# Kernel tuning notes

Hardware: AMD Instinct MI355X
Metric: run time of the kernel (lower is better)

Reference implementation:

```python
import jax, jax.numpy as jnp
import numpy as np

B, N, D = 16, 4096, 128
M = 2048  # codebook size
EPS = 1e-10


def setup_inputs() -> dict:
    key = jax.random.key(0)
    kx, kw = jax.random.split(key)
    x = jax.random.normal(kx, (B, N, D), dtype=jnp.float32)
    # codebook (nn.Embedding weight, kaiming-uniform init ~ uniform(-bound, bound))
    bound = np.sqrt(6.0 / D)
    weight = jax.random.uniform(kw, (M, D), dtype=jnp.float32, minval=-bound, maxval=bound)
    return {"x": x, "weight": weight}


def reference(x, weight):
    b, n, d = x.shape
    m = weight.shape[0]
    q = x.reshape(b * n, d)                       # (bn, d)
    # squared L2 distances: ||q||^2 + ||k||^2 - 2 q.k  (temperature==0 -> argmax of -dist)
    l2_q = jnp.sum(q * q, axis=1, keepdims=True)  # (bn, 1)
    l2_k = jnp.sum(weight * weight, axis=1)       # (m,)
    sim = q @ weight.T                            # (bn, m)  GEMM
    dist = l2_q + l2_k - 2.0 * sim
    indices = jnp.argmin(dist, axis=1)            # (bn,)
    z = weight[indices]                           # onehot @ k == gather
    quantized = z.reshape(b, n, d)
    # straight-through estimator (training path): q + (z - q).detach()
    quantized_st = x + jax.lax.stop_gradient(quantized - x)
    # commitment loss: mse(quantized.detach(), x)
    loss = jnp.mean((jax.lax.stop_gradient(quantized_st) - x) ** 2)
    # perplexity over codebook usage (h == 1 head)
    counts = jnp.zeros((m,), dtype=x.dtype).at[indices].add(1.0)
    p = counts / (b * n)                          # mean of onehot over (b, n)
    perp = jnp.exp(-jnp.sum(p * jnp.log(p + EPS)))[None]  # shape (1,) == 'h'
    out_indices = indices.reshape(b, 1, n)
    return quantized_st, loss, perp, out_indices
```

## Files before the change

### kernel.cpp

```cpp
#include <hip/hip_runtime.h>
#include <hip/hip_bf16.h>
#include <math.h>

#define D_DIM 128
#define M_CODES 2048
#define BN_TOT 65536
#define OUT_LOSS 8388608
#define OUT_PERP 8388609
#define OUT_IDX 8388610
#define MARGIN 2e-3f

#define QB 32

#define WS_L2K 0
#define WS_PHI 8192
#define WS_PLO 532480
#define WS_IDX 1056768
#define WS_PART 1318912
#define WS_CNT 1351680
#define WS_FLAGCNT 1359872
#define WS_FLAGGED 1360896

typedef __bf16 bf16x8 __attribute__((ext_vector_type(8)));
typedef float f32x4 __attribute__((ext_vector_type(4)));

#define A_STRIDE 136

__global__ __launch_bounds__(256) void l2_kernel(const float* __restrict__ w,
                                                 float* __restrict__ l2k) {
  int i = blockIdx.x * 256 + threadIdx.x;
  const float4* p = (const float4*)(w + (size_t)i * D_DIM);
  double s = 0.0;
#pragma unroll
  for (int j = 0; j < 32; ++j) {
    float4 v = p[j];
    s += (double)(v.x * v.x);
    s += (double)(v.y * v.y);
    s += (double)(v.z * v.z);
    s += (double)(v.w * v.w);
  }
  l2k[i] = (float)s;
}

__global__ __launch_bounds__(256) void pack_w_frag(const float* __restrict__ w,
                                                   __bf16* __restrict__ phi,
                                                   __bf16* __restrict__ plo) {
  int gid = blockIdx.x * 256 + threadIdx.x;
  int lane = gid & 63;
  int t = gid >> 6;
  int nt = t & 3;
  int ks = (t >> 2) & 3;
  int c64 = t >> 4;
  int code = c64 * 64 + nt * 16 + (lane & 15);
  int koff = ks * 32 + (lane >> 4) * 8;
  const float* src = w + (size_t)code * D_DIM + koff;
  float4 u = *(const float4*)src;
  float4 v = *(const float4*)(src + 4);
  float f[8] = {u.x, u.y, u.z, u.w, v.x, v.y, v.z, v.w};
  bf16x8 h, l;
#pragma unroll
  for (int j = 0; j < 8; ++j) {
    __bf16 hh = (__bf16)f[j];
    h[j] = hh;
    l[j] = (__bf16)(f[j] - (float)hh);
  }
  *(bf16x8*)(phi + (size_t)gid * 8) = h;
  *(bf16x8*)(plo + (size_t)gid * 8) = l;
}

__device__ __forceinline__ void merge_bs(float& b, float& s, int& i,
                                         float ob, float os, int oi) {
  if (ob < b) {
    s = fminf(b, os);
    b = ob;
    i = oi;
  } else if (ob > b) {
    s = fminf(s, ob);
  } else {
    s = b;
    if (oi < i) i = oi;
  }
}

__global__ __launch_bounds__(256, 1) void argmin_mfma(
    const float* __restrict__ x, const __bf16* __restrict__ phi,
    const __bf16* __restrict__ plo, const float* __restrict__ l2k,
    int* __restrict__ best_idx, int* __restrict__ flag_count,
    int* __restrict__ flagged) {
  __shared__ __bf16 aHi[QB * A_STRIDE];
  __shared__ __bf16 aLo[QB * A_STRIDE];
  __shared__ float redB[4][QB];
  __shared__ float redS[4][QB];
  __shared__ int redI[4][QB];

  const int tid = threadIdx.x;
  const int q0 = blockIdx.x * QB;
  const int wv = tid >> 6;
  const int lane = tid & 63;
  const int col = lane & 15;
  const int quad = lane >> 4;

#pragma unroll
  for (int it = 0; it < 4; ++it) {
    int fid = tid + it * 256;
    int q = fid >> 5;
    int k4 = (fid & 31) * 4;
    float4 v = *(const float4*)(x + (size_t)(q0 + q) * D_DIM + k4);
    float f[4] = {v.x, v.y, v.z, v.w};
    int base = q * A_STRIDE + k4;
#pragma unroll
    for (int j = 0; j < 4; ++j) {
      __bf16 h = (__bf16)f[j];
      aHi[base + j] = h;
      aLo[base + j] = (__bf16)(f[j] - (float)h);
    }
  }
  __syncthreads();

  float m1[2][4], m2[2][4];
  int bi[2][4];
#pragma unroll
  for (int mt = 0; mt < 2; ++mt)
#pragma unroll
    for (int r = 0; r < 4; ++r) {
      m1[mt][r] = 3.4e38f;
      m2[mt][r] = 3.4e38f;
      bi[mt][r] = 0;
    }

  for (int ch = 0; ch < 8; ++ch) {
    const int cb = ch * 256 + wv * 64;
    const int cb64 = ch * 4 + wv;

    bf16x8 bh[4][4], bl[4][4];
#pragma unroll
    for (int ks = 0; ks < 4; ++ks) {
#pragma unroll
      for (int nt = 0; nt < 4; ++nt) {
        size_t g = (((size_t)cb64 * 16) + ks * 4 + nt) * 64 + lane;
        bh[ks][nt] = *(const bf16x8*)(phi + g * 8);
        bl[ks][nt] = *(const bf16x8*)(plo + g * 8);
      }
    }

    f32x4 acc[2][4];
#pragma unroll
    for (int mt = 0; mt < 2; ++mt)
#pragma unroll
      for (int nt = 0; nt < 4; ++nt) acc[mt][nt] = (f32x4){0.f, 0.f, 0.f, 0.f};

#pragma unroll
    for (int ks = 0; ks < 4; ++ks) {
      bf16x8 ah[2], al[2];
#pragma unroll
      for (int mt = 0; mt < 2; ++mt) {
        int off = (16 * mt + col) * A_STRIDE + 32 * ks + quad * 8;
        ah[mt] = *(const bf16x8*)&aHi[off];
        al[mt] = *(const bf16x8*)&aLo[off];
      }
#pragma unroll
      for (int nt = 0; nt < 4; ++nt) {
#pragma unroll
        for (int mt = 0; mt < 2; ++mt) {
          acc[mt][nt] = __builtin_amdgcn_mfma_f32_16x16x32_bf16(
              al[mt], bh[ks][nt], acc[mt][nt], 0, 0, 0);
          acc[mt][nt] = __builtin_amdgcn_mfma_f32_16x16x32_bf16(
              ah[mt], bl[ks][nt], acc[mt][nt], 0, 0, 0);
          acc[mt][nt] = __builtin_amdgcn_mfma_f32_16x16x32_bf16(
              ah[mt], bh[ks][nt], acc[mt][nt], 0, 0, 0);
        }
      }
    }

#pragma unroll
    for (int nt = 0; nt < 4; ++nt) {
      int ci = cb + 16 * nt + col;
      float l2 = l2k[ci];
#pragma unroll
      for (int mt = 0; mt < 2; ++mt) {
#pragma unroll
        for (int r = 0; r < 4; ++r) {
          float dd = fmaf(-2.0f, acc[mt][nt][r], l2);
          bool lt = dd < m1[mt][r];
          m2[mt][r] = lt ? m1[mt][r] : fminf(m2[mt][r], dd);
          bi[mt][r] = lt ? ci : bi[mt][r];
          m1[mt][r] = fminf(m1[mt][r], dd);
        }
      }
    }
  }

#pragma unroll
  for (int mt = 0; mt < 2; ++mt) {
#pragma unroll
    for (int r = 0; r < 4; ++r) {
      float b = m1[mt][r], s = m2[mt][r];
      int i = bi[mt][r];
#pragma unroll
      for (int m = 1; m < 16; m <<= 1) {
        float ob = __shfl_xor(b, m);
        float os = __shfl_xor(s, m);
        int oi = __shfl_xor(i, m);
        merge_bs(b, s, i, ob, os, oi);
      }
      if (col == 0) {
        int qloc = 16 * mt + 4 * quad + r;
        redB[wv][qloc] = b;
        redS[wv][qloc] = s;
        redI[wv][qloc] = i;
      }
    }
  }
  __syncthreads();

  if (tid < QB) {
    float b = 3.4e38f, s = 3.4e38f;
    int i = 0x7fffffff;
#pragma unroll
    for (int w4 = 0; w4 < 4; ++w4)
      merge_bs(b, s, i, redB[w4][tid], redS[w4][tid], redI[w4][tid]);
    best_idx[q0 + tid] = i;
    if (s - b < MARGIN) {
      int pos = atomicAdd(flag_count, 1);
      flagged[pos] = q0 + tid;
    }
  }
}

__global__ __launch_bounds__(256) void fixup_kernel(const float* __restrict__ x,
                                                    const float* __restrict__ w,
                                                    const float* __restrict__ l2k32,
                                                    const int* __restrict__ flagged,
                                                    const int* __restrict__ flag_count,
                                                    int* __restrict__ best_idx) {
  __shared__ float qs[D_DIM];
  __shared__ float l2q_sh;
  __shared__ float redD[256];
  __shared__ int redI[256];
  const int tid = threadIdx.x;
  const int n = *flag_count;
  for (int f = blockIdx.x; f < n; f += gridDim.x) {
    __syncthreads();
    int q = flagged[f];
    if (tid < D_DIM) qs[tid] = x[(size_t)q * D_DIM + tid];
    __syncthreads();
    if (tid == 0) {
      double s = 0.0;
      for (int d = 0; d < D_DIM; ++d) {
        float t = qs[d] * qs[d];
        s += (double)t;
      }
      l2q_sh = (float)s;
    }
    __syncthreads();
    const float l2q = l2q_sh;
    float bd = 3.4e38f;
    int bi = 0x7fffffff;
    for (int c = tid; c < M_CODES; c += 256) {
      const float4* wr = (const float4*)(w + (size_t)c * D_DIM);
      double s = 0.0;
#pragma unroll
      for (int j = 0; j < 32; ++j) {
        float4 v = wr[j];
        s = fma((double)qs[j * 4 + 0], (double)v.x, s);
        s = fma((double)qs[j * 4 + 1], (double)v.y, s);
        s = fma((double)qs[j * 4 + 2], (double)v.z, s);
        s = fma((double)qs[j * 4 + 3], (double)v.w, s);
      }
      float simf = (float)s;
      float S = l2q + l2k32[c];
      float T = 2.0f * simf;
      float dist = S - T;
      if (dist < bd) { bd = dist; bi = c; }
    }
    redD[tid] = bd;
    redI[tid] = bi;
    __syncthreads();
    for (int off = 128; off; off >>= 1) {
      if (tid < off) {
        float od = redD[tid + off];
        int oi = redI[tid + off];
        if (od < redD[tid] || (od == redD[tid] && oi < redI[tid])) {
          redD[tid] = od;
          redI[tid] = oi;
        }
      }
      __syncthreads();
    }
    if (tid == 0) best_idx[q] = redI[0];
  }
}

__global__ __launch_bounds__(256) void epilogue_kernel(const float* __restrict__ x,
                                                       const float* __restrict__ w,
                                                       const int* __restrict__ best_idx,
                                                       float* __restrict__ out,
                                                       float* __restrict__ part,
                                                       int* __restrict__ counts) {
  int gid = blockIdx.x * 256 + threadIdx.x;
  int q = gid >> 5;
  int d4 = gid & 31;
  int idx = best_idx[q];
  float4 xv = ((const float4*)x)[gid];
  float4 wv = ((const float4*)w)[(size_t)idx * 32 + d4];
  float4 o;
  float t0 = wv.x - xv.x; o.x = xv.x + t0; float e0 = o.x - xv.x;
  float t1 = wv.y - xv.y; o.y = xv.y + t1; float e1 = o.y - xv.y;
  float t2 = wv.z - xv.z; o.z = xv.z + t2; float e2 = o.z - xv.z;
  float t3 = wv.w - xv.w; o.w = xv.w + t3; float e3 = o.w - xv.w;
  float ls = e0 * e0 + e1 * e1 + e2 * e2 + e3 * e3;
  ((float4*)out)[gid] = o;

  for (int off = 32; off; off >>= 1) ls += __shfl_down(ls, off);
  __shared__ float red[4];
  if ((threadIdx.x & 63) == 0) red[threadIdx.x >> 6] = ls;
  __syncthreads();
  if (threadIdx.x == 0) part[blockIdx.x] = red[0] + red[1] + red[2] + red[3];

  if (d4 == 0) {
    out[OUT_IDX + q] = (float)idx;
    atomicAdd(&counts[idx], 1);
  }
}

__global__ __launch_bounds__(256) void finalize_kernel(const int* __restrict__ counts,
                                                       const float* __restrict__ part,
                                                       float* __restrict__ out) {
  int tid = threadIdx.x;
  float ls = 0.f;
  for (int i = tid; i < 8192; i += 256) ls += part[i];
  float es = 0.f;
  for (int i = tid; i < M_CODES; i += 256) {
    float p = (float)counts[i] * (1.0f / 65536.0f);
    es += p * logf(p + 1e-10f);
  }
  for (int off = 32; off; off >>= 1) {
    ls += __shfl_down(ls, off);
    es += __shfl_down(es, off);
  }
  __shared__ float redl[4], rede[4];
  if ((tid & 63) == 0) {
    redl[tid >> 6] = ls;
    rede[tid >> 6] = es;
  }
  __syncthreads();
  if (tid == 0) {
    out[OUT_LOSS] = (redl[0] + redl[1] + redl[2] + redl[3]) * (1.0f / 8388608.0f);
    out[OUT_PERP] = expf(-(rede[0] + rede[1] + rede[2] + rede[3]));
  }
}

extern "C" void kernel_launch(void* const* d_in, const int* in_sizes, int n_in,
                              void* d_out, int out_size, void* d_ws, size_t ws_size,
                              hipStream_t stream) {
  const float* x = (const float*)d_in[0];
  const float* w = (const float*)d_in[1];
  float* out = (float*)d_out;
  char* ws = (char*)d_ws;
  float* l2k = (float*)(ws + WS_L2K);
  __bf16* phi = (__bf16*)(ws + WS_PHI);
  __bf16* plo = (__bf16*)(ws + WS_PLO);
  int* bidx = (int*)(ws + WS_IDX);
  float* part = (float*)(ws + WS_PART);
  int* counts = (int*)(ws + WS_CNT);
  int* flagcnt = (int*)(ws + WS_FLAGCNT);
  int* flagged = (int*)(ws + WS_FLAGGED);

  hipMemsetAsync(counts, 0, M_CODES * sizeof(int), stream);
  hipMemsetAsync(flagcnt, 0, sizeof(int), stream);
  l2_kernel<<<8, 256, 0, stream>>>(w, l2k);
  pack_w_frag<<<128, 256, 0, stream>>>(w, phi, plo);
  argmin_mfma<<<BN_TOT / QB, 256, 0, stream>>>(x, phi, plo, l2k, bidx, flagcnt, flagged);
  fixup_kernel<<<256, 256, 0, stream>>>(x, w, l2k, flagged, flagcnt, bidx);
  epilogue_kernel<<<8192, 256, 0, stream>>>(x, w, bidx, out, part, counts);
  finalize_kernel<<<1, 256, 0, stream>>>(counts, part, out);
}
```

Before: 277.3 us.

## Stage codebook tiles through double-buffered LDS with async global-to-LDS loads

The argmin kernel now processes 64 queries per block, split across 2x2 waves, and keeps the query hi/lo bf16 fragments in registers instead of LDS. Codebook fragments are streamed in 32-code chunks into double-buffered LDS with global_load_lds, so the next chunk's load overlaps the current chunk's MFMAs and two waves share each staged tile. This cuts redundant global reads of the codebook and lets up to 3 blocks per CU fit. In exchange it adds a block-wide barrier on every one of 64 iterations and does less MFMA work per barrier.

```diff
diff --git a/kernel.cpp b/kernel.cpp
--- a/kernel.cpp
+++ b/kernel.cpp
@@ -10,7 +10,7 @@
 #define OUT_IDX 8388610
 #define MARGIN 2e-3f
 
-#define QB 32
+#define QB 64
 
 #define WS_L2K 0
 #define WS_PHI 8192
@@ -24,7 +24,10 @@
 typedef __bf16 bf16x8 __attribute__((ext_vector_type(8)));
 typedef float f32x4 __attribute__((ext_vector_type(4)));
 
-#define A_STRIDE 136
+#define GLOAD_LDS16(g, l)                                         \
+  __builtin_amdgcn_global_load_lds(                               \
+      (const __attribute__((address_space(1))) void*)(g),         \
+      (__attribute__((address_space(3))) void*)(l), 16, 0, 0)
 
 __global__ __launch_bounds__(256) void l2_kernel(const float* __restrict__ w,
                                                  float* __restrict__ l2k) {
@@ -82,40 +85,46 @@
   }
 }
 
-__global__ __launch_bounds__(256, 1) void argmin_mfma(
+__global__ __launch_bounds__(256, 3) void argmin_mfma(
     const float* __restrict__ x, const __bf16* __restrict__ phi,
     const __bf16* __restrict__ plo, const float* __restrict__ l2k,
     int* __restrict__ best_idx, int* __restrict__ flag_count,
     int* __restrict__ flagged) {
-  __shared__ __bf16 aHi[QB * A_STRIDE];
-  __shared__ __bf16 aLo[QB * A_STRIDE];
-  __shared__ float redB[4][QB];
-  __shared__ float redS[4][QB];
-  __shared__ int redI[4][QB];
+  __shared__ __align__(16) unsigned char ldsB[2][16 * 1024];
+  __shared__ float redB[4][32];
+  __shared__ float redS[4][32];
+  __shared__ int redI[4][32];
 
   const int tid = threadIdx.x;
-  const int q0 = blockIdx.x * QB;
   const int wv = tid >> 6;
   const int lane = tid & 63;
   const int col = lane & 15;
   const int quad = lane >> 4;
-
-#pragma unroll
-  for (int it = 0; it < 4; ++it) {
-    int fid = tid + it * 256;
-    int q = fid >> 5;
-    int k4 = (fid & 31) * 4;
-    float4 v = *(const float4*)(x + (size_t)(q0 + q) * D_DIM + k4);
-    float f[4] = {v.x, v.y, v.z, v.w};
-    int base = q * A_STRIDE + k4;
-#pragma unroll
-    for (int j = 0; j < 4; ++j) {
-      __bf16 h = (__bf16)f[j];
-      aHi[base + j] = h;
-      aLo[base + j] = (__bf16)(f[j] - (float)h);
-    }
-  }
-  __syncthreads();
+  const int wc = wv & 1;
+  const int wq = wv >> 1;
+  const int q0 = blockIdx.x * QB;
+
+  bf16x8 ah[2][4], al[2][4];
+#pragma unroll
+  for (int mt = 0; mt < 2; ++mt) {
+#pragma unroll
+    for (int ks = 0; ks < 4; ++ks) {
+      const float* xr =
+          x + (size_t)(q0 + wq * 32 + 16 * mt + col) * D_DIM + 32 * ks + 8 * quad;
+      float4 u = *(const float4*)xr;
+      float4 v = *(const float4*)(xr + 4);
+      float f[8] = {u.x, u.y, u.z, u.w, v.x, v.y, v.z, v.w};
+      bf16x8 h, l;
+#pragma unroll
+      for (int j = 0; j < 8; ++j) {
+        __bf16 hh = (__bf16)f[j];
+        h[j] = hh;
+        l[j] = (__bf16)(f[j] - (float)hh);
+      }
+      ah[mt][ks] = h;
+      al[mt][ks] = l;
+    }
+  }
 
   float m1[2][4], m2[2][4];
   int bi[2][4];
@@ -128,66 +137,57 @@
       bi[mt][r] = 0;
     }
 
-  for (int ch = 0; ch < 8; ++ch) {
-    const int cb = ch * 256 + wv * 64;
-    const int cb64 = ch * 4 + wv;
-
-    bf16x8 bh[4][4], bl[4][4];
+  auto stage = [&](int ch, int buf) {
+    const int c64 = ch >> 1;
+    const int ntb = (ch & 1) * 2;
+#pragma unroll
+    for (int i = 0; i < 4; ++i) {
+      int cid = wv * 4 + i;
+      int k2 = cid & 7;
+      int gran = c64 * 16 + (k2 >> 1) * 4 + ntb + (k2 & 1);
+      const __bf16* src = (cid < 8 ? phi : plo) + (size_t)gran * 512 + lane * 8;
+      GLOAD_LDS16(src, &ldsB[buf][cid * 1024]);
+    }
+  };
+
+  stage(0, 0);
+  __syncthreads();
+
+  for (int ch = 0; ch < 64; ++ch) {
+    const int buf = ch & 1;
+    if (ch < 63) stage(ch + 1, buf ^ 1);
+
+    f32x4 acc[2];
+#pragma unroll
+    for (int mt = 0; mt < 2; ++mt) acc[mt] = (f32x4){0.f, 0.f, 0.f, 0.f};
+
 #pragma unroll
     for (int ks = 0; ks < 4; ++ks) {
-#pragma unroll
-      for (int nt = 0; nt < 4; ++nt) {
-        size_t g = (((size_t)cb64 * 16) + ks * 4 + nt) * 64 + lane;
-        bh[ks][nt] = *(const bf16x8*)(phi + g * 8);
-        bl[ks][nt] = *(const bf16x8*)(plo + g * 8);
-      }
-    }
-
-    f32x4 acc[2][4];
-#pragma unroll
-    for (int mt = 0; mt < 2; ++mt)
-#pragma unroll
-      for (int nt = 0; nt < 4; ++nt) acc[mt][nt] = (f32x4){0.f, 0.f, 0.f, 0.f};
-
-#pragma unroll
-    for (int ks = 0; ks < 4; ++ks) {
-      bf16x8 ah[2], al[2];
+      bf16x8 bh = *(const bf16x8*)&ldsB[buf][(ks * 2 + wc) * 1024 + lane * 16];
+      bf16x8 bl = *(const bf16x8*)&ldsB[buf][(8 + ks * 2 + wc) * 1024 + lane * 16];
 #pragma unroll
       for (int mt = 0; mt < 2; ++mt) {
-        int off = (16 * mt + col) * A_STRIDE + 32 * ks + quad * 8;
-        ah[mt] = *(const bf16x8*)&aHi[off];
-        al[mt] = *(const bf16x8*)&aLo[off];
-      }
-#pragma unroll
-      for (int nt = 0; nt < 4; ++nt) {
-#pragma unroll
-        for (int mt = 0; mt < 2; ++mt) {
-          acc[mt][nt] = __builtin_amdgcn_mfma_f32_16x16x32_bf16(
-              al[mt], bh[ks][nt], acc[mt][nt], 0, 0, 0);
-          acc[mt][nt] = __builtin_amdgcn_mfma_f32_16x16x32_bf16(
-              ah[mt], bl[ks][nt], acc[mt][nt], 0, 0, 0);
-          acc[mt][nt] = __builtin_amdgcn_mfma_f32_16x16x32_bf16(
-              ah[mt], bh[ks][nt], acc[mt][nt], 0, 0, 0);
-        }
-      }
-    }
-
-#pragma unroll
-    for (int nt = 0; nt < 4; ++nt) {
-      int ci = cb + 16 * nt + col;
-      float l2 = l2k[ci];
-#pragma unroll
-      for (int mt = 0; mt < 2; ++mt) {
-#pragma unroll
-        for (int r = 0; r < 4; ++r) {
-          float dd = fmaf(-2.0f, acc[mt][nt][r], l2);
-          bool lt = dd < m1[mt][r];
-          m2[mt][r] = lt ? m1[mt][r] : fminf(m2[mt][r], dd);
-          bi[mt][r] = lt ? ci : bi[mt][r];
-          m1[mt][r] = fminf(m1[mt][r], dd);
-        }
-      }
-    }
+        acc[mt] = __builtin_amdgcn_mfma_f32_16x16x32_bf16(al[mt][ks], bh, acc[mt], 0, 0, 0);
+        acc[mt] = __builtin_amdgcn_mfma_f32_16x16x32_bf16(ah[mt][ks], bl, acc[mt], 0, 0, 0);
+        acc[mt] = __builtin_amdgcn_mfma_f32_16x16x32_bf16(ah[mt][ks], bh, acc[mt], 0, 0, 0);
+      }
+    }
+
+    const int ci = ch * 32 + wc * 16 + col;
+    const float l2 = l2k[ci];
+#pragma unroll
+    for (int mt = 0; mt < 2; ++mt) {
+#pragma unroll
+      for (int r = 0; r < 4; ++r) {
+        float dd = fmaf(-2.0f, acc[mt][r], l2);
+        bool lt = dd < m1[mt][r];
+        m2[mt][r] = lt ? m1[mt][r] : fminf(m2[mt][r], dd);
+        bi[mt][r] = lt ? ci : bi[mt][r];
+        m1[mt][r] = fminf(m1[mt][r], dd);
+      }
+    }
+
+    __syncthreads();
   }
 
 #pragma unroll
@@ -214,11 +214,12 @@
   __syncthreads();
 
   if (tid < QB) {
+    int wq2 = tid >> 5;
+    int ql = tid & 31;
     float b = 3.4e38f, s = 3.4e38f;
     int i = 0x7fffffff;
-#pragma unroll
-    for (int w4 = 0; w4 < 4; ++w4)
-      merge_bs(b, s, i, redB[w4][tid], redS[w4][tid], redI[w4][tid]);
+    merge_bs(b, s, i, redB[wq2 * 2 + 0][ql], redS[wq2 * 2 + 0][ql], redI[wq2 * 2 + 0][ql]);
+    merge_bs(b, s, i, redB[wq2 * 2 + 1][ql], redS[wq2 * 2 + 1][ql], redI[wq2 * 2 + 1][ql]);
     best_idx[q0 + tid] = i;
     if (s - b < MARGIN) {
       int pos = atomicAdd(flag_count, 1);
```

After: 251.9 us. -9.2%, faster.
